# Kernel optimization log

Measured on AMD Instinct MI355X. Metric: run time of the kernel, lower is better.

Reference implementation:

```python
import jax, jax.numpy as jnp
import numpy as np

WINDOW = 7
NUM_HEADS = 16
HEAD_DIM = 32  # dim 512 / 16 heads
SCALE = HEAD_DIM ** -0.5


def _relative_position_index(ws: int) -> np.ndarray:
    coords = np.stack(np.meshgrid(np.arange(ws), np.arange(ws), indexing='ij'))  # [2, ws, ws]
    flat = coords.reshape(2, -1)  # [2, N]
    rel = flat[:, :, None] - flat[:, None, :]  # [2, N, N]
    rel = rel.transpose(1, 2, 0)  # [N, N, 2]
    rh = (rel[:, :, 0] + ws - 1) * (2 * ws - 1)
    rw = rel[:, :, 1] + ws - 1
    return (rh + rw).astype(np.int32)  # [N, N]

REL_IDX = jnp.asarray(_relative_position_index(WINDOW))  # [49, 49]


def setup_inputs() -> dict:
    key = jax.random.key(0)
    ks = jax.random.split(key, 4)
    B, N, C = 4096, WINDOW * WINDOW, 512
    x = jax.random.normal(ks[0], (B, N, C), dtype=jnp.float32)
    qkv_w = jax.random.normal(ks[1], (C, 3 * C), dtype=jnp.float32) * (C ** -0.5)
    qkv_b = jnp.zeros((3 * C,), dtype=jnp.float32)
    proj_w = jax.random.normal(ks[2], (C, C), dtype=jnp.float32) * (C ** -0.5)
    proj_b = jnp.zeros((C,), dtype=jnp.float32)
    bias_table = jax.random.normal(ks[3], ((2 * WINDOW - 1) ** 2, NUM_HEADS), dtype=jnp.float32) * 0.02
    return {"x": x, "qkv_w": qkv_w, "qkv_b": qkv_b, "proj_w": proj_w,
            "proj_b": proj_b, "bias_table": bias_table}


def reference(x, qkv_w, qkv_b, proj_w, proj_b, bias_table):
    B, N, C = x.shape
    # QKV projection -> [B, N, 3, H, D] -> q/k/v [B, H, N, D]
    qkv = (x @ qkv_w + qkv_b).reshape(B, N, 3, NUM_HEADS, HEAD_DIM)
    qkv = jnp.transpose(qkv, (2, 0, 3, 1, 4))
    q, k, v = qkv[0], qkv[1], qkv[2]
    attn = jnp.einsum('bhnd,bhmd->bhnm', q * SCALE, k)  # [B, H, N, N]
    # relative position bias gather: [N*N, H] -> [1, H, N, N]
    bias = bias_table[REL_IDX.reshape(-1)].reshape(N, N, NUM_HEADS)
    attn = attn + jnp.transpose(bias, (2, 0, 1))[None]
    attn = jax.nn.softmax(attn, axis=-1)
    out = jnp.einsum('bhnm,bhmd->bhnd', attn, v)  # [B, H, N, D]
    out = jnp.transpose(out, (0, 2, 1, 3)).reshape(B, N, C)
    return out @ proj_w + proj_b
```

## Files before the change

kernel.cpp:

```cpp
#include <hip/hip_runtime.h>

typedef _Float16 h16;
typedef __attribute__((ext_vector_type(4))) _Float16 h16x4;
typedef __attribute__((ext_vector_type(8))) _Float16 h16x8;
typedef __attribute__((ext_vector_type(4))) float f32x4;

#define SCALE 0.17677669529663687f
#define MFMA16(a, b, c) __builtin_amdgcn_mfma_f32_16x16x16f16(a, b, c, 0, 0, 0)
#define MFMA32(a, b, c) __builtin_amdgcn_mfma_f32_16x16x32_f16(a, b, c, 0, 0, 0)

#define O_BYTES 205520896ULL
#define W1F_OFF (O_BYTES)
#define W2T_OFF (W1F_OFF + 1572864ULL)
#define BT_OFF  (W2T_OFF + 524288ULL)

__global__ __launch_bounds__(256) void wa_pack_w1(
    const float* __restrict__ qkv_w, h16* __restrict__ w1F) {
  int chunk = blockIdx.x * 256 + threadIdx.x;
  int lane = chunk & 63;
  int rest = chunk >> 6;
  int f  = rest % 12;
  int kt = (rest / 12) & 7;
  int wv = (rest / 96) & 3;
  int g  = rest / 384;
  int s = f >> 2, d = (f >> 1) & 1, ks = f & 1;
  int l15 = lane & 15, lg = lane >> 4;
  int o = s * 512 + g * 128 + wv * 32 + d * 16 + l15;
  int k0 = kt * 64 + ks * 32 + lg * 8;
  float sc = (s == 0) ? SCALE : 1.0f;
  h16x8 v;
  #pragma unroll
  for (int e = 0; e < 8; ++e)
    v[e] = (h16)(qkv_w[(size_t)(k0 + e) * 1536 + o] * sc);
  *(h16x8*)(w1F + (size_t)chunk * 8) = v;
}

__global__ __launch_bounds__(256) void wa_transpose_w2(
    const float* __restrict__ proj_w, h16* __restrict__ w2T) {
  __shared__ h16 T[32][33];
  int tx = threadIdx.x & 31, ty = threadIdx.x >> 5;
  int bo = blockIdx.x & 15, bc = blockIdx.x >> 4;
  #pragma unroll
  for (int i = 0; i < 4; ++i) {
    int c = bc * 32 + ty + 8 * i, o = bo * 32 + tx;
    T[ty + 8 * i][tx] = (h16)proj_w[c * 512 + o];
  }
  __syncthreads();
  #pragma unroll
  for (int i = 0; i < 4; ++i) {
    int o_l = ty + 8 * i;
    w2T[(size_t)(bo * 32 + o_l) * 512 + bc * 32 + tx] = T[tx][o_l];
  }
}

__global__ __launch_bounds__(256) void wa_build_bias(
    const float* __restrict__ table, float* __restrict__ biasT) {
  int idx = blockIdx.x * 256 + threadIdx.x;
  int h = idx >> 12, q = (idx >> 6) & 63, j = idx & 63;
  float v = -1e30f;
  if (j < 49 && q < 49) {
    int rel = (q / 7 - j / 7 + 6) * 13 + (q % 7 - j % 7 + 6);
    v = table[rel * 16 + h];
  }
  biasT[idx] = v;
}

__global__ __launch_bounds__(256, 2) void wa_qkv_attn(
    const float* __restrict__ x, const float* __restrict__ qkv_b,
    const h16* __restrict__ w1F, const float* __restrict__ biasT,
    h16* __restrict__ O) {
  __shared__ __align__(16) char lds[65536];
  const int tid = threadIdx.x;
  const int wave = tid >> 6, lane = tid & 63;
  const int l15 = lane & 15, lg = lane >> 4;
  const int sw = l15 & 7;
  const int lbid = (blockIdx.x & 7) * 2048 + (blockIdx.x >> 3);
  const int w = lbid >> 2, g = lbid & 3;
  const int head = g * 4 + wave;
  const size_t rowbase = (size_t)w * 49;

  #pragma unroll
  for (int p = 0; p < 13; ++p) {
    int idx = tid + p * 256;
    if (idx < 3136) {
      int r = idx >> 6, c = idx & 63;
      const float* src = x + (rowbase + r) * 512 + c * 8;
      float4 a = *(const float4*)(src);
      float4 b = *(const float4*)(src + 4);
      h16x8 h = { (h16)a.x, (h16)a.y, (h16)a.z, (h16)a.w,
                  (h16)b.x, (h16)b.y, (h16)b.z, (h16)b.w };
      *(h16x8*)(lds + r * 1024 + ((c ^ (r & 7)) << 4)) = h;
    }
  }
  #pragma unroll
  for (int p = 0; p < 4; ++p) {
    int idx = tid + p * 256;
    if (idx < 960) {
      int r = 49 + (idx >> 6), c = idx & 63;
      *(h16x8*)(lds + r * 1024 + ((c ^ (r & 7)) << 4)) = (h16x8){0,0,0,0,0,0,0,0};
    }
  }
  __syncthreads();

  f32x4 accQ[2][4], accK[2][4], accV[4][2];
  #pragma unroll
  for (int d = 0; d < 2; ++d)
    #pragma unroll
    for (int t = 0; t < 4; ++t) {
      accQ[d][t] = (f32x4){0.f, 0.f, 0.f, 0.f};
      accK[d][t] = (f32x4){0.f, 0.f, 0.f, 0.f};
      accV[t][d] = (f32x4){0.f, 0.f, 0.f, 0.f};
    }

  const h16* wb = w1F + ((size_t)(g * 4 + wave) * 8) * 6144 + lane * 8;
  int xb[4];
  #pragma unroll
  for (int t = 0; t < 4; ++t) xb[t] = (16 * t + l15) * 1024;
  const int co0 = ((lg) ^ sw) << 4, co1 = ((4 + lg) ^ sw) << 4;
  const h16x4 ones = (h16x4){(h16)1.f, (h16)1.f, (h16)1.f, (h16)1.f};

  h16x8 WA[12], WB[12];
#define WLOAD(DST, KT) {                                                   \
    _Pragma("unroll") for (int f = 0; f < 12; ++f)                         \
      DST[f] = *(const h16x8*)(wb + (size_t)(KT) * 6144 + f * 512); }

#define GSTEP(KT, W) {                                                     \
    h16x8 xf[4];                                                           \
    _Pragma("unroll") for (int t = 0; t < 4; ++t)                          \
      xf[t] = *(const h16x8*)(lds + xb[t] + co0 + (KT) * 128);             \
    __builtin_amdgcn_s_setprio(1);                                         \
    _Pragma("unroll") for (int d = 0; d < 2; ++d)                          \
    _Pragma("unroll") for (int t = 0; t < 4; ++t) {                        \
      accQ[d][t] = MFMA32(W[0 + d*2], xf[t], accQ[d][t]);                  \
      accK[d][t] = MFMA32(W[4 + d*2], xf[t], accK[d][t]);                  \
      accV[t][d] = MFMA32(xf[t], W[8 + d*2], accV[t][d]);                  \
    }                                                                      \
    __builtin_amdgcn_s_setprio(0);                                         \
    _Pragma("unroll") for (int t = 0; t < 4; ++t)                          \
      xf[t] = *(const h16x8*)(lds + xb[t] + co1 + (KT) * 128);             \
    __builtin_amdgcn_s_setprio(1);                                         \
    _Pragma("unroll") for (int d = 0; d < 2; ++d)                          \
    _Pragma("unroll") for (int t = 0; t < 4; ++t) {                        \
      accQ[d][t] = MFMA32(W[1 + d*2], xf[t], accQ[d][t]);                  \
      accK[d][t] = MFMA32(W[5 + d*2], xf[t], accK[d][t]);                  \
      accV[t][d] = MFMA32(xf[t], W[9 + d*2], accV[t][d]);                  \
    }                                                                      \
    __builtin_amdgcn_s_setprio(0); }

  WLOAD(WA, 0);
  for (int kt2 = 0; kt2 < 4; ++kt2) {
    WLOAD(WB, 2 * kt2 + 1);
    GSTEP(2 * kt2, WA);
    if (kt2 < 3) WLOAD(WA, 2 * kt2 + 2);
    GSTEP(2 * kt2 + 1, WB);
  }
#undef WLOAD
#undef GSTEP

  float bq[2][4], bk[2][4], bv[2];
  #pragma unroll
  for (int d = 0; d < 2; ++d) {
    #pragma unroll
    for (int r = 0; r < 4; ++r) {
      bq[d][r] = qkv_b[head * 32 + 16 * d + 4 * lg + r] * SCALE;
      bk[d][r] = qkv_b[512 + head * 32 + 16 * d + 4 * lg + r];
    }
    bv[d] = qkv_b[1024 + head * 32 + 16 * d + l15];
  }
  const float* bT = biasT + head * 4096;

  h16x4 Qh[2][4], Kh[2][4], Vh[4][2];
  #pragma unroll
  for (int d = 0; d < 2; ++d)
    #pragma unroll
    for (int t = 0; t < 4; ++t)
      #pragma unroll
      for (int r = 0; r < 4; ++r) {
        Qh[d][t][r] = (h16)(accQ[d][t][r] + bq[d][r]);
        Kh[d][t][r] = (h16)(accK[d][t][r] + bk[d][r]);
        Vh[t][d][r] = (h16)(accV[t][d][r] + bv[d]);
      }

  f32x4 st[4][4];
  #pragma unroll
  for (int a = 0; a < 4; ++a)
    #pragma unroll
    for (int b = 0; b < 4; ++b) st[a][b] = (f32x4){0.f, 0.f, 0.f, 0.f};
  __builtin_amdgcn_s_setprio(1);
  #pragma unroll
  for (int d = 0; d < 2; ++d)
    #pragma unroll
    for (int jt = 0; jt < 4; ++jt)
      #pragma unroll
      for (int qt = 0; qt < 4; ++qt)
        st[jt][qt] = MFMA16(Kh[d][jt], Qh[d][qt], st[jt][qt]);
  __builtin_amdgcn_s_setprio(0);

  h16x4 pf[4][4];
  #pragma unroll
  for (int qt = 0; qt < 4; ++qt) {
    int q = 16 * qt + l15;
    #pragma unroll
    for (int jt = 0; jt < 4; ++jt) {
      float4 bvv = *(const float4*)(bT + q * 64 + 16 * jt + 4 * lg);
      h16x4 p;
      #pragma unroll
      for (int r = 0; r < 4; ++r)
        p[r] = (h16)__expf(st[jt][qt][r] + ((const float*)&bvv)[r]);
      pf[jt][qt] = p;
    }
  }

  f32x4 ss[4];
  #pragma unroll
  for (int qt = 0; qt < 4; ++qt) ss[qt] = (f32x4){0.f, 0.f, 0.f, 0.f};
  f32x4 ot[2][4];
  #pragma unroll
  for (int d = 0; d < 2; ++d)
    #pragma unroll
    for (int qt = 0; qt < 4; ++qt) ot[d][qt] = (f32x4){0.f, 0.f, 0.f, 0.f};
  __builtin_amdgcn_s_setprio(1);
  #pragma unroll
  for (int jt = 0; jt < 4; ++jt)
    #pragma unroll
    for (int qt = 0; qt < 4; ++qt) {
      ss[qt] = MFMA16(ones, pf[jt][qt], ss[qt]);
      #pragma unroll
      for (int d = 0; d < 2; ++d)
        ot[d][qt] = MFMA16(Vh[jt][d], pf[jt][qt], ot[d][qt]);
    }
  __builtin_amdgcn_s_setprio(0);

  #pragma unroll
  for (int qt = 0; qt < 4; ++qt) {
    int q = 16 * qt + l15;
    float ri = 1.0f / ss[qt][0];
    if (q < 49) {
      h16* gdst = O + (rowbase + q) * 512 + head * 32 + 4 * lg;
      #pragma unroll
      for (int d = 0; d < 2; ++d) {
        h16x4 ov;
        #pragma unroll
        for (int r = 0; r < 4; ++r) ov[r] = (h16)(ot[d][qt][r] * ri);
        *(h16x4*)(gdst + 16 * d) = ov;
      }
    }
  }
}

__global__ __launch_bounds__(256, 3) void wa_proj(
    const h16* __restrict__ O, const h16* __restrict__ w2T,
    const float* __restrict__ proj_b, float* __restrict__ out) {
  __shared__ __align__(16) char lds[32768];
  char* Ac = lds;
  char* Bc = lds + 16384;
  const int tid = threadIdx.x;
  const int wave = tid >> 6, lane = tid & 63;
  const int l15 = lane & 15, lg = lane >> 4;
  const int lbid = (blockIdx.x & 7) * 784 + (blockIdx.x >> 3);
  const int rowt = lbid >> 2, colt = lbid & 3;
  const int wr = wave >> 1, wc = wave & 1;

  f32x4 acc[4][4];
  #pragma unroll
  for (int a = 0; a < 4; ++a)
    #pragma unroll
    for (int b = 0; b < 4; ++b) acc[a][b] = (f32x4){0.f, 0.f, 0.f, 0.f};

  h16x8 pre[8];
  #pragma unroll
  for (int p = 0; p < 8; ++p) {
    int idx = tid + p * 256;
    int r = (idx >> 3) & 127, c = idx & 7;
    pre[p] = (idx < 1024)
        ? *(const h16x8*)(O   + (size_t)(rowt * 128 + r) * 512 + c * 8)
        : *(const h16x8*)(w2T + (size_t)(colt * 128 + r) * 512 + c * 8);
  }
  #pragma unroll
  for (int p = 0; p < 8; ++p) {
    int idx = tid + p * 256;
    int r = (idx >> 3) & 127, c = idx & 7;
    char* dst = ((idx < 1024) ? Ac : Bc) + r * 128 + ((c ^ (r & 7)) << 4);
    *(h16x8*)dst = pre[p];
  }
  __syncthreads();

  for (int kt = 0; kt < 8; ++kt) {
    if (kt < 7) {
      #pragma unroll
      for (int p = 0; p < 8; ++p) {
        int idx = tid + p * 256;
        int r = (idx >> 3) & 127, c = idx & 7;
        pre[p] = (idx < 1024)
            ? *(const h16x8*)(O   + (size_t)(rowt * 128 + r) * 512 + (kt + 1) * 64 + c * 8)
            : *(const h16x8*)(w2T + (size_t)(colt * 128 + r) * 512 + (kt + 1) * 64 + c * 8);
      }
    }
    #pragma unroll
    for (int kh = 0; kh < 2; ++kh) {
      const int cc = kh * 4 + lg;
      const int sw = (l15 & 7);
      h16x8 af[4], bf[4];
      #pragma unroll
      for (int mt = 0; mt < 4; ++mt) {
        int r = wr * 64 + 16 * mt + l15;
        af[mt] = *(const h16x8*)(Ac + r * 128 + ((cc ^ sw) << 4));
      }
      #pragma unroll
      for (int nt = 0; nt < 4; ++nt) {
        int r = wc * 64 + 16 * nt + l15;
        bf[nt] = *(const h16x8*)(Bc + r * 128 + ((cc ^ sw) << 4));
      }
      __builtin_amdgcn_s_setprio(1);
      #pragma unroll
      for (int mt = 0; mt < 4; ++mt)
        #pragma unroll
        for (int nt = 0; nt < 4; ++nt)
          acc[mt][nt] = MFMA32(af[mt], bf[nt], acc[mt][nt]);
      __builtin_amdgcn_s_setprio(0);
    }
    __syncthreads();
    if (kt < 7) {
      #pragma unroll
      for (int p = 0; p < 8; ++p) {
        int idx = tid + p * 256;
        int r = (idx >> 3) & 127, c = idx & 7;
        char* dst = ((idx < 1024) ? Ac : Bc) + r * 128 + ((c ^ (r & 7)) << 4);
        *(h16x8*)dst = pre[p];
      }
      __syncthreads();
    }
  }
  #pragma unroll
  for (int nt = 0; nt < 4; ++nt) {
    int col = colt * 128 + wc * 64 + nt * 16 + l15;
    float pb = proj_b[col];
    #pragma unroll
    for (int mt = 0; mt < 4; ++mt) {
      int row = rowt * 128 + wr * 64 + mt * 16 + 4 * lg;
      #pragma unroll
      for (int r = 0; r < 4; ++r)
        out[(size_t)(row + r) * 512 + col] = acc[mt][nt][r] + pb;
    }
  }
}

extern "C" void kernel_launch(void* const* d_in, const int* in_sizes, int n_in,
                              void* d_out, int out_size, void* d_ws, size_t ws_size,
                              hipStream_t stream) {
  const float* x          = (const float*)d_in[0];
  const float* qkv_w      = (const float*)d_in[1];
  const float* qkv_b      = (const float*)d_in[2];
  const float* proj_w     = (const float*)d_in[3];
  const float* proj_b     = (const float*)d_in[4];
  const float* bias_table = (const float*)d_in[5];
  float* out = (float*)d_out;

  char* ws = (char*)d_ws;
  h16*   O     = (h16*)ws;
  h16*   w1F   = (h16*)(ws + W1F_OFF);
  h16*   w2T   = (h16*)(ws + W2T_OFF);
  float* biasT = (float*)(ws + BT_OFF);

  wa_pack_w1<<<384, 256, 0, stream>>>(qkv_w, w1F);
  wa_transpose_w2<<<256, 256, 0, stream>>>(proj_w, w2T);
  wa_build_bias<<<256, 256, 0, stream>>>(bias_table, biasT);
  wa_qkv_attn<<<4096 * 4, 256, 0, stream>>>(x, qkv_b, w1F, biasT, O);
  wa_proj<<<1568 * 4, 256, 0, stream>>>(O, w2T, proj_b, out);
}
```

Measured before the change: 774.3 us.

## Process two head groups per block to reuse staged x tile, merge prep kernels

The attention kernel now handles two head groups per block, looping over them after staging the window's x tile in LDS once. This halves the grid and halves the redundant global reads and fp16 conversion of x. The three weight and bias prep kernels are merged into one launch. The bias table is stored in MFMA fragment order and pre-scaled by log2(e), with log2(e) folded into the Q scale so the softmax can use exp2f. The cost is fewer blocks and a longer serial body per block, which may reduce latency hiding.

```diff
diff --git a/kernel.cpp b/kernel.cpp
--- a/kernel.cpp
+++ b/kernel.cpp
@@ -5,78 +5,85 @@
 typedef __attribute__((ext_vector_type(8))) _Float16 h16x8;
 typedef __attribute__((ext_vector_type(4))) float f32x4;
 
-#define SCALE 0.17677669529663687f
+#define QSCALE 0.25505653882616254f
+#define LOG2E  1.4426950408889634f
 #define MFMA16(a, b, c) __builtin_amdgcn_mfma_f32_16x16x16f16(a, b, c, 0, 0, 0)
 #define MFMA32(a, b, c) __builtin_amdgcn_mfma_f32_16x16x32_f16(a, b, c, 0, 0, 0)
 
 #define O_BYTES 205520896ULL
 #define W1F_OFF (O_BYTES)
 #define W2T_OFF (W1F_OFF + 1572864ULL)
-#define BT_OFF  (W2T_OFF + 524288ULL)
-
-__global__ __launch_bounds__(256) void wa_pack_w1(
-    const float* __restrict__ qkv_w, h16* __restrict__ w1F) {
-  int chunk = blockIdx.x * 256 + threadIdx.x;
-  int lane = chunk & 63;
-  int rest = chunk >> 6;
-  int f  = rest % 12;
-  int kt = (rest / 12) & 7;
-  int wv = (rest / 96) & 3;
-  int g  = rest / 384;
-  int s = f >> 2, d = (f >> 1) & 1, ks = f & 1;
-  int l15 = lane & 15, lg = lane >> 4;
-  int o = s * 512 + g * 128 + wv * 32 + d * 16 + l15;
-  int k0 = kt * 64 + ks * 32 + lg * 8;
-  float sc = (s == 0) ? SCALE : 1.0f;
-  h16x8 v;
-  #pragma unroll
-  for (int e = 0; e < 8; ++e)
-    v[e] = (h16)(qkv_w[(size_t)(k0 + e) * 1536 + o] * sc);
-  *(h16x8*)(w1F + (size_t)chunk * 8) = v;
-}
-
-__global__ __launch_bounds__(256) void wa_transpose_w2(
-    const float* __restrict__ proj_w, h16* __restrict__ w2T) {
+#define BF_OFF  (W2T_OFF + 524288ULL)
+
+__global__ __launch_bounds__(256) void wa_prep(
+    const float* __restrict__ qkv_w, const float* __restrict__ proj_w,
+    const float* __restrict__ table,
+    h16* __restrict__ w1F, h16* __restrict__ w2T, float* __restrict__ biasF) {
   __shared__ h16 T[32][33];
-  int tx = threadIdx.x & 31, ty = threadIdx.x >> 5;
-  int bo = blockIdx.x & 15, bc = blockIdx.x >> 4;
-  #pragma unroll
-  for (int i = 0; i < 4; ++i) {
-    int c = bc * 32 + ty + 8 * i, o = bo * 32 + tx;
-    T[ty + 8 * i][tx] = (h16)proj_w[c * 512 + o];
-  }
-  __syncthreads();
-  #pragma unroll
-  for (int i = 0; i < 4; ++i) {
-    int o_l = ty + 8 * i;
-    w2T[(size_t)(bo * 32 + o_l) * 512 + bc * 32 + tx] = T[tx][o_l];
-  }
-}
-
-__global__ __launch_bounds__(256) void wa_build_bias(
-    const float* __restrict__ table, float* __restrict__ biasT) {
-  int idx = blockIdx.x * 256 + threadIdx.x;
-  int h = idx >> 12, q = (idx >> 6) & 63, j = idx & 63;
-  float v = -1e30f;
-  if (j < 49 && q < 49) {
-    int rel = (q / 7 - j / 7 + 6) * 13 + (q % 7 - j % 7 + 6);
-    v = table[rel * 16 + h];
-  }
-  biasT[idx] = v;
+  const int b = blockIdx.x, tid = threadIdx.x;
+  if (b < 256) {
+    int tx = tid & 31, ty = tid >> 5;
+    int bo = b & 15, bc = b >> 4;
+    #pragma unroll
+    for (int i = 0; i < 4; ++i) {
+      int c = bc * 32 + ty + 8 * i, o = bo * 32 + tx;
+      T[ty + 8 * i][tx] = (h16)proj_w[c * 512 + o];
+    }
+    __syncthreads();
+    #pragma unroll
+    for (int i = 0; i < 4; ++i) {
+      int o_l = ty + 8 * i;
+      w2T[(size_t)(bo * 32 + o_l) * 512 + bc * 32 + tx] = T[tx][o_l];
+    }
+  } else if (b < 640) {
+    int chunk = (b - 256) * 256 + tid;
+    int lane = chunk & 63;
+    int rest = chunk >> 6;
+    int f  = rest % 12;
+    int kt = (rest / 12) & 7;
+    int wv = (rest / 96) & 3;
+    int g  = rest / 384;
+    int s = f >> 2, d = (f >> 1) & 1, ks = f & 1;
+    int l15 = lane & 15, lg = lane >> 4;
+    int o = s * 512 + g * 128 + wv * 32 + d * 16 + l15;
+    int k0 = kt * 64 + ks * 32 + lg * 8;
+    float sc = (s == 0) ? QSCALE : 1.0f;
+    h16x8 v;
+    #pragma unroll
+    for (int e = 0; e < 8; ++e)
+      v[e] = (h16)(qkv_w[(size_t)(k0 + e) * 1536 + o] * sc);
+    *(h16x8*)(w1F + (size_t)chunk * 8) = v;
+  } else {
+    int t = (b - 640) * 256 + tid;
+    int lane = t & 63, jt = (t >> 6) & 3, qt = (t >> 8) & 3, head = t >> 10;
+    int l15 = lane & 15, lg = lane >> 4;
+    int q = qt * 16 + l15;
+    float4 v;
+    #pragma unroll
+    for (int r = 0; r < 4; ++r) {
+      int j = jt * 16 + lg * 4 + r;
+      float val = -1e30f;
+      if (j < 49 && q < 49) {
+        int rel = (q / 7 - j / 7 + 6) * 13 + (q % 7 - j % 7 + 6);
+        val = table[rel * 16 + head] * LOG2E;
+      }
+      ((float*)&v)[r] = val;
+    }
+    ((float4*)biasF)[t] = v;
+  }
 }
 
 __global__ __launch_bounds__(256, 2) void wa_qkv_attn(
     const float* __restrict__ x, const float* __restrict__ qkv_b,
-    const h16* __restrict__ w1F, const float* __restrict__ biasT,
+    const h16* __restrict__ w1F, const float* __restrict__ biasF,
     h16* __restrict__ O) {
   __shared__ __align__(16) char lds[65536];
   const int tid = threadIdx.x;
   const int wave = tid >> 6, lane = tid & 63;
   const int l15 = lane & 15, lg = lane >> 4;
   const int sw = l15 & 7;
-  const int lbid = (blockIdx.x & 7) * 2048 + (blockIdx.x >> 3);
-  const int w = lbid >> 2, g = lbid & 3;
-  const int head = g * 4 + wave;
+  const int lbid = (blockIdx.x & 7) * 1024 + (blockIdx.x >> 3);
+  const int w = lbid >> 1, gp = lbid & 1;
   const size_t rowbase = (size_t)w * 49;
 
   #pragma unroll
@@ -86,9 +93,9 @@
       int r = idx >> 6, c = idx & 63;
       const float* src = x + (rowbase + r) * 512 + c * 8;
       float4 a = *(const float4*)(src);
-      float4 b = *(const float4*)(src + 4);
+      float4 bb = *(const float4*)(src + 4);
       h16x8 h = { (h16)a.x, (h16)a.y, (h16)a.z, (h16)a.w,
-                  (h16)b.x, (h16)b.y, (h16)b.z, (h16)b.w };
+                  (h16)bb.x, (h16)bb.y, (h16)bb.z, (h16)bb.w };
       *(h16x8*)(lds + r * 1024 + ((c ^ (r & 7)) << 4)) = h;
     }
   }
@@ -102,24 +109,13 @@
   }
   __syncthreads();
 
-  f32x4 accQ[2][4], accK[2][4], accV[4][2];
-  #pragma unroll
-  for (int d = 0; d < 2; ++d)
-    #pragma unroll
-    for (int t = 0; t < 4; ++t) {
-      accQ[d][t] = (f32x4){0.f, 0.f, 0.f, 0.f};
-      accK[d][t] = (f32x4){0.f, 0.f, 0.f, 0.f};
-      accV[t][d] = (f32x4){0.f, 0.f, 0.f, 0.f};
-    }
-
-  const h16* wb = w1F + ((size_t)(g * 4 + wave) * 8) * 6144 + lane * 8;
   int xb[4];
   #pragma unroll
   for (int t = 0; t < 4; ++t) xb[t] = (16 * t + l15) * 1024;
   const int co0 = ((lg) ^ sw) << 4, co1 = ((4 + lg) ^ sw) << 4;
   const h16x4 ones = (h16x4){(h16)1.f, (h16)1.f, (h16)1.f, (h16)1.f};
-
-  h16x8 WA[12], WB[12];
+  const float4* bF4 = (const float4*)biasF;
+
 #define WLOAD(DST, KT) {                                                   \
     _Pragma("unroll") for (int f = 0; f < 12; ++f)                         \
       DST[f] = *(const h16x8*)(wb + (size_t)(KT) * 6144 + f * 512); }
@@ -147,105 +143,93 @@
     }                                                                      \
     __builtin_amdgcn_s_setprio(0); }
 
-  WLOAD(WA, 0);
-  for (int kt2 = 0; kt2 < 4; ++kt2) {
-    WLOAD(WB, 2 * kt2 + 1);
-    GSTEP(2 * kt2, WA);
-    if (kt2 < 3) WLOAD(WA, 2 * kt2 + 2);
-    GSTEP(2 * kt2 + 1, WB);
-  }
+#define PROCESS_HEAD(G) {                                                  \
+    const int head = (G) * 4 + wave;                                       \
+    const h16* wb = w1F + ((size_t)((G) * 4 + wave) * 8) * 6144 + lane * 8;\
+    f32x4 accQ[2][4], accK[2][4], accV[4][2];                              \
+    _Pragma("unroll") for (int d = 0; d < 2; ++d)                          \
+    _Pragma("unroll") for (int t = 0; t < 4; ++t) {                        \
+      accQ[d][t] = (f32x4){0.f, 0.f, 0.f, 0.f};                            \
+      accK[d][t] = (f32x4){0.f, 0.f, 0.f, 0.f};                            \
+      accV[t][d] = (f32x4){0.f, 0.f, 0.f, 0.f};                            \
+    }                                                                      \
+    h16x8 WA[12], WB[12];                                                  \
+    WLOAD(WA, 0);                                                          \
+    for (int kt2 = 0; kt2 < 4; ++kt2) {                                    \
+      WLOAD(WB, 2 * kt2 + 1);                                              \
+      GSTEP(2 * kt2, WA);                                                  \
+      if (kt2 < 3) WLOAD(WA, 2 * kt2 + 2);                                 \
+      GSTEP(2 * kt2 + 1, WB);                                              \
+    }                                                                      \
+    float bq[2][4], bk[2][4], bv[2];                                       \
+    _Pragma("unroll") for (int d = 0; d < 2; ++d) {                        \
+      _Pragma("unroll") for (int r = 0; r < 4; ++r) {                      \
+        bq[d][r] = qkv_b[head * 32 + 16 * d + 4 * lg + r] * QSCALE;        \
+        bk[d][r] = qkv_b[512 + head * 32 + 16 * d + 4 * lg + r];           \
+      }                                                                    \
+      bv[d] = qkv_b[1024 + head * 32 + 16 * d + l15];                      \
+    }                                                                      \
+    h16x4 Qh[2][4], Kh[2][4], Vh[4][2];                                    \
+    _Pragma("unroll") for (int d = 0; d < 2; ++d)                          \
+    _Pragma("unroll") for (int t = 0; t < 4; ++t)                          \
+    _Pragma("unroll") for (int r = 0; r < 4; ++r) {                        \
+      Qh[d][t][r] = (h16)(accQ[d][t][r] + bq[d][r]);                       \
+      Kh[d][t][r] = (h16)(accK[d][t][r] + bk[d][r]);                       \
+      Vh[t][d][r] = (h16)(accV[t][d][r] + bv[d]);                          \
+    }                                                                      \
+    f32x4 st[4][4];                                                        \
+    _Pragma("unroll") for (int a = 0; a < 4; ++a)                          \
+    _Pragma("unroll") for (int bb = 0; bb < 4; ++bb)                       \
+      st[a][bb] = (f32x4){0.f, 0.f, 0.f, 0.f};                             \
+    __builtin_amdgcn_s_setprio(1);                                         \
+    _Pragma("unroll") for (int d = 0; d < 2; ++d)                          \
+    _Pragma("unroll") for (int jt = 0; jt < 4; ++jt)                       \
+    _Pragma("unroll") for (int qt = 0; qt < 4; ++qt)                       \
+      st[jt][qt] = MFMA16(Kh[d][jt], Qh[d][qt], st[jt][qt]);               \
+    __builtin_amdgcn_s_setprio(0);                                         \
+    h16x4 pf[4][4];                                                        \
+    _Pragma("unroll") for (int qt = 0; qt < 4; ++qt)                       \
+    _Pragma("unroll") for (int jt = 0; jt < 4; ++jt) {                     \
+      float4 bvv = bF4[(head * 16 + qt * 4 + jt) * 64 + lane];             \
+      h16x4 p;                                                             \
+      _Pragma("unroll") for (int r = 0; r < 4; ++r)                        \
+        p[r] = (h16)exp2f(st[jt][qt][r] + ((const float*)&bvv)[r]);        \
+      pf[jt][qt] = p;                                                      \
+    }                                                                      \
+    f32x4 ss[4];                                                           \
+    _Pragma("unroll") for (int qt = 0; qt < 4; ++qt)                       \
+      ss[qt] = (f32x4){0.f, 0.f, 0.f, 0.f};                                \
+    f32x4 ot[2][4];                                                        \
+    _Pragma("unroll") for (int d = 0; d < 2; ++d)                          \
+    _Pragma("unroll") for (int qt = 0; qt < 4; ++qt)                       \
+      ot[d][qt] = (f32x4){0.f, 0.f, 0.f, 0.f};                             \
+    __builtin_amdgcn_s_setprio(1);                                         \
+    _Pragma("unroll") for (int jt = 0; jt < 4; ++jt)                       \
+    _Pragma("unroll") for (int qt = 0; qt < 4; ++qt) {                     \
+      ss[qt] = MFMA16(ones, pf[jt][qt], ss[qt]);                           \
+      _Pragma("unroll") for (int d = 0; d < 2; ++d)                        \
+        ot[d][qt] = MFMA16(Vh[jt][d], pf[jt][qt], ot[d][qt]);              \
+    }                                                                      \
+    __builtin_amdgcn_s_setprio(0);                                         \
+    _Pragma("unroll") for (int qt = 0; qt < 4; ++qt) {                     \
+      int q = 16 * qt + l15;                                               \
+      float ri = 1.0f / ss[qt][0];                                         \
+      if (q < 49) {                                                        \
+        h16* gdst = O + (rowbase + q) * 512 + head * 32 + 4 * lg;          \
+        _Pragma("unroll") for (int d = 0; d < 2; ++d) {                    \
+          h16x4 ov;                                                        \
+          _Pragma("unroll") for (int r = 0; r < 4; ++r)                    \
+            ov[r] = (h16)(ot[d][qt][r] * ri);                              \
+          *(h16x4*)(gdst + 16 * d) = ov;                                   \
+        }                                                                  \
+      }                                                                    \
+    } }
+
+  PROCESS_HEAD(gp * 2);
+  PROCESS_HEAD(gp * 2 + 1);
+#undef PROCESS_HEAD
 #undef WLOAD
 #undef GSTEP
-
-  float bq[2][4], bk[2][4], bv[2];
-  #pragma unroll
-  for (int d = 0; d < 2; ++d) {
-    #pragma unroll
-    for (int r = 0; r < 4; ++r) {
-      bq[d][r] = qkv_b[head * 32 + 16 * d + 4 * lg + r] * SCALE;
-      bk[d][r] = qkv_b[512 + head * 32 + 16 * d + 4 * lg + r];
-    }
-    bv[d] = qkv_b[1024 + head * 32 + 16 * d + l15];
-  }
-  const float* bT = biasT + head * 4096;
-
-  h16x4 Qh[2][4], Kh[2][4], Vh[4][2];
-  #pragma unroll
-  for (int d = 0; d < 2; ++d)
-    #pragma unroll
-    for (int t = 0; t < 4; ++t)
-      #pragma unroll
-      for (int r = 0; r < 4; ++r) {
-        Qh[d][t][r] = (h16)(accQ[d][t][r] + bq[d][r]);
-        Kh[d][t][r] = (h16)(accK[d][t][r] + bk[d][r]);
-        Vh[t][d][r] = (h16)(accV[t][d][r] + bv[d]);
-      }
-
-  f32x4 st[4][4];
-  #pragma unroll
-  for (int a = 0; a < 4; ++a)
-    #pragma unroll
-    for (int b = 0; b < 4; ++b) st[a][b] = (f32x4){0.f, 0.f, 0.f, 0.f};
-  __builtin_amdgcn_s_setprio(1);
-  #pragma unroll
-  for (int d = 0; d < 2; ++d)
-    #pragma unroll
-    for (int jt = 0; jt < 4; ++jt)
-      #pragma unroll
-      for (int qt = 0; qt < 4; ++qt)
-        st[jt][qt] = MFMA16(Kh[d][jt], Qh[d][qt], st[jt][qt]);
-  __builtin_amdgcn_s_setprio(0);
-
-  h16x4 pf[4][4];
-  #pragma unroll
-  for (int qt = 0; qt < 4; ++qt) {
-    int q = 16 * qt + l15;
-    #pragma unroll
-    for (int jt = 0; jt < 4; ++jt) {
-      float4 bvv = *(const float4*)(bT + q * 64 + 16 * jt + 4 * lg);
-      h16x4 p;
-      #pragma unroll
-      for (int r = 0; r < 4; ++r)
-        p[r] = (h16)__expf(st[jt][qt][r] + ((const float*)&bvv)[r]);
-      pf[jt][qt] = p;
-    }
-  }
-
-  f32x4 ss[4];
-  #pragma unroll
-  for (int qt = 0; qt < 4; ++qt) ss[qt] = (f32x4){0.f, 0.f, 0.f, 0.f};
-  f32x4 ot[2][4];
-  #pragma unroll
-  for (int d = 0; d < 2; ++d)
-    #pragma unroll
-    for (int qt = 0; qt < 4; ++qt) ot[d][qt] = (f32x4){0.f, 0.f, 0.f, 0.f};
-  __builtin_amdgcn_s_setprio(1);
-  #pragma unroll
-  for (int jt = 0; jt < 4; ++jt)
-    #pragma unroll
-    for (int qt = 0; qt < 4; ++qt) {
-      ss[qt] = MFMA16(ones, pf[jt][qt], ss[qt]);
-      #pragma unroll
-      for (int d = 0; d < 2; ++d)
-        ot[d][qt] = MFMA16(Vh[jt][d], pf[jt][qt], ot[d][qt]);
-    }
-  __builtin_amdgcn_s_setprio(0);
-
-  #pragma unroll
-  for (int qt = 0; qt < 4; ++qt) {
-    int q = 16 * qt + l15;
-    float ri = 1.0f / ss[qt][0];
-    if (q < 49) {
-      h16* gdst = O + (rowbase + q) * 512 + head * 32 + 4 * lg;
-      #pragma unroll
-      for (int d = 0; d < 2; ++d) {
-        h16x4 ov;
-        #pragma unroll
-        for (int r = 0; r < 4; ++r) ov[r] = (h16)(ot[d][qt][r] * ri);
-        *(h16x4*)(gdst + 16 * d) = ov;
-      }
-    }
-  }
 }
 
 __global__ __launch_bounds__(256, 3) void wa_proj(
@@ -360,11 +344,9 @@
   h16*   O     = (h16*)ws;
   h16*   w1F   = (h16*)(ws + W1F_OFF);
   h16*   w2T   = (h16*)(ws + W2T_OFF);
-  float* biasT = (float*)(ws + BT_OFF);
-
-  wa_pack_w1<<<384, 256, 0, stream>>>(qkv_w, w1F);
-  wa_transpose_w2<<<256, 256, 0, stream>>>(proj_w, w2T);
-  wa_build_bias<<<256, 256, 0, stream>>>(bias_table, biasT);
-  wa_qkv_attn<<<4096 * 4, 256, 0, stream>>>(x, qkv_b, w1F, biasT, O);
+  float* biasF = (float*)(ws + BF_OFF);
+
+  wa_prep<<<704, 256, 0, stream>>>(qkv_w, proj_w, bias_table, w1F, w2T, biasF);
+  wa_qkv_attn<<<8192, 256, 0, stream>>>(x, qkv_b, w1F, biasF, O);
   wa_proj<<<1568 * 4, 256, 0, stream>>>(O, w2T, proj_b, out);
 }
```

Measured after the change: 691.0 us. -10.8%, faster.
